# Performance work log

Hardware: AMD Instinct MI355X
Metric: run time of the kernel (lower is better)

The kernel has to match this reference:

```python
import jax, jax.numpy as jnp
import numpy as np

N, H, W, C = 2, 96, 96, 256
HEADS, P = 8, 25
DH = C // HEADS
HID = int(C * 4.0)


def _ln(x, g, b):
    m = jnp.mean(x, axis=-1, keepdims=True)
    v = jnp.var(x, axis=-1, keepdims=True)
    return (x - m) / jnp.sqrt(v + 1e-5) * g + b


def _deform_sample(value, loc, h, w):
    # value: (n, heads, h*w, dh); loc: (n, Lq, heads, P, 2) normalized to [0,1] (x,y)
    # Bilinear sampling with align_corners=False and zero padding, as in
    # grid_sample used by MSDeformAttn.
    n = value.shape[0]
    gx = loc[..., 0] * w - 0.5
    gy = loc[..., 1] * h - 0.5
    x0 = jnp.floor(gx)
    y0 = jnp.floor(gy)
    fx = gx - x0
    fy = gy - y0
    out = jnp.zeros((n, HEADS, gx.shape[1] * P, DH), dtype=value.dtype)
    for dx, dy in ((0, 0), (1, 0), (0, 1), (1, 1)):
        xi = x0 + dx
        yi = y0 + dy
        wgt = (fx if dx else 1.0 - fx) * (fy if dy else 1.0 - fy)
        valid = ((xi >= 0) & (xi <= w - 1) & (yi >= 0) & (yi <= h - 1)).astype(value.dtype)
        xi_c = jnp.clip(xi, 0, w - 1).astype(jnp.int32)
        yi_c = jnp.clip(yi, 0, h - 1).astype(jnp.int32)
        idx = yi_c * w + xi_c                                   # (n, Lq, heads, P)
        idx = jnp.transpose(idx, (0, 2, 1, 3)).reshape(n, HEADS, -1)
        g = jnp.take_along_axis(value, idx[..., None], axis=2)  # (n, heads, Lq*P, dh)
        wv = jnp.transpose(wgt * valid, (0, 2, 1, 3)).reshape(n, HEADS, -1, 1)
        out = out + g * wv
    return out


def setup_inputs() -> dict:
    key = jax.random.key(0)
    ks = jax.random.split(key, 20)
    s = 0.02
    inp = {
        'x': jax.random.normal(ks[0], (N, H, W, C), jnp.float32),
        'ref_points': jax.random.uniform(ks[1], (N, H * W, 1, 2), jnp.float32),
        'spatial_shapes': jnp.array([[H, W]], dtype=jnp.int32),
        'level_start_index': jnp.zeros((1,), dtype=jnp.int32),
        'ln1_g': jnp.ones((C,), jnp.float32),
        'ln1_b': jnp.zeros((C,), jnp.float32),
        'w_off': jax.random.normal(ks[2], (C, HEADS * P * 2), jnp.float32) * s,
        'b_off': jax.random.normal(ks[3], (HEADS * P * 2,), jnp.float32) * s,
        'w_attn': jax.random.normal(ks[4], (C, HEADS * P), jnp.float32) * s,
        'b_attn': jax.random.normal(ks[5], (HEADS * P,), jnp.float32) * s,
        'w_val': jax.random.normal(ks[6], (C, C), jnp.float32) * s,
        'b_val': jnp.zeros((C,), jnp.float32),
        'w_out': jax.random.normal(ks[7], (C, C), jnp.float32) * s,
        'b_out': jnp.zeros((C,), jnp.float32),
        'ln2_g': jnp.ones((C,), jnp.float32),
        'ln2_b': jnp.zeros((C,), jnp.float32),
        'w_fc1': jax.random.normal(ks[8], (C, HID), jnp.float32) * s,
        'b_fc1': jnp.zeros((HID,), jnp.float32),
        'w_fc2': jax.random.normal(ks[9], (HID, C), jnp.float32) * s,
        'b_fc2': jnp.zeros((C,), jnp.float32),
    }
    return inp


def reference(x, ref_points, spatial_shapes, level_start_index,
              ln1_g, ln1_b, w_off, b_off, w_attn, b_attn,
              w_val, b_val, w_out, b_out, ln2_g, ln2_b,
              w_fc1, b_fc1, w_fc2, b_fc2):
    n, h, w, c = x.shape
    lq = h * w
    shortcut = x
    # pre-norm + flatten to query
    q = _ln(x, ln1_g, ln1_b).reshape(n, lq, c)
    # MSDeformAttn (n_levels = 1)
    value = (q @ w_val + b_val).reshape(n, lq, HEADS, DH).transpose(0, 2, 1, 3)
    off = (q @ w_off + b_off).reshape(n, lq, HEADS, P, 2)
    aw = jax.nn.softmax((q @ w_attn + b_attn).reshape(n, lq, HEADS, P), axis=-1)
    norm = jnp.array([w, h], dtype=x.dtype)          # offsets normalized by (W, H)
    ref = ref_points[:, :, 0, :]                     # (n, Lq, 2)
    loc = ref[:, :, None, None, :] + off / norm      # (n, Lq, heads, P, 2)
    sampled = _deform_sample(value, loc, h, w).reshape(n, HEADS, lq, P, DH)
    attn = jnp.einsum('nqhp,nhqpd->nqhd', aw, sampled).reshape(n, lq, c)
    attn = attn @ w_out + b_out
    x1 = shortcut + attn.reshape(n, h, w, c)
    # MLP block
    y = _ln(x1, ln2_g, ln2_b)
    y = jax.nn.gelu(y @ w_fc1 + b_fc1, approximate=False) @ w_fc2 + b_fc2
    return x1 + y
```

## Files before the change

### kernel.cpp

```cpp
#include <hip/hip_runtime.h>
#include <hip/hip_bf16.h>
#include <math.h>

typedef __hip_bfloat16 bf16;
typedef __attribute__((ext_vector_type(8))) short short8;
typedef __attribute__((ext_vector_type(4))) float f32x4;

#define NB 2
#define HH 96
#define WW 96
#define CC 256
#define NHEADS 8
#define PP 25
#define DHH 32
#define HIDN 1024
#define LQ (HH*WW)
#define TT (NB*LQ)
#define NVC 896
#define TB 8

__device__ __forceinline__ float b2f(bf16 v){ return __bfloat162float(v); }
__device__ __forceinline__ bf16  f2b(float v){ return __float2bfloat16(v); }
__device__ __forceinline__ float lo_bf(unsigned u){ return __uint_as_float(u << 16); }
__device__ __forceinline__ float hi_bf(unsigned u){ return __uint_as_float(u & 0xffff0000u); }

__device__ __forceinline__ void gl2lds16(const void* g, void* l) {
    __builtin_amdgcn_global_load_lds(
        (const __attribute__((address_space(1))) unsigned int*)g,
        (__attribute__((address_space(3))) unsigned int*)l, 16, 0, 0);
}

__global__ __launch_bounds__(256) void prep_all(const float* __restrict__ w_val,
                                                const float* __restrict__ w_off,
                                                const float* __restrict__ w_attn,
                                                const float* __restrict__ w_fc1,
                                                const float* __restrict__ w_fc2,
                                                const float* __restrict__ w_out,
                                                const float* __restrict__ b_val,
                                                const float* __restrict__ b_off,
                                                const float* __restrict__ b_attn,
                                                bf16* __restrict__ wvcT,
                                                bf16* __restrict__ wfc1T,
                                                bf16* __restrict__ wfc2T,
                                                bf16* __restrict__ woutT,
                                                float* __restrict__ bvc)
{
    const int idx = blockIdx.x*256 + threadIdx.x;
    if (idx < 229376) {
        int n = idx >> 8, k = idx & 255;
        float v = (n < 256) ? w_val[(size_t)k*256 + n]
                : (n < 656) ? w_off[(size_t)k*400 + (n-256)]
                : (n < 856) ? w_attn[(size_t)k*200 + (n-656)] : 0.f;
        wvcT[idx] = f2b(v);
    } else if (idx < 491520) {
        int j = idx - 229376; int n = j >> 8, k = j & 255;
        wfc1T[j] = f2b(w_fc1[(size_t)k*1024 + n]);
    } else if (idx < 753664) {
        int j = idx - 491520; int n = j >> 10, k = j & 1023;
        wfc2T[j] = f2b(w_fc2[(size_t)k*256 + n]);
    } else if (idx < 819200) {
        int j = idx - 753664; int n = j >> 8, k = j & 255;
        woutT[j] = f2b(w_out[(size_t)k*256 + n]);
    }
    if (idx < NVC)
        bvc[idx] = (idx < 256) ? b_val[idx]
                 : (idx < 656) ? b_off[idx-256]
                 : (idx < 856) ? b_attn[idx-656] : 0.f;
}

__global__ __launch_bounds__(256) void ln_kernel(const float* __restrict__ x,
                                                 const float* __restrict__ g,
                                                 const float* __restrict__ b,
                                                 bf16* __restrict__ out)
{
    const int t = blockIdx.x*4 + (threadIdx.x >> 6);
    const int l = threadIdx.x & 63;
    const float4 v = *(const float4*)(x + (size_t)t*CC + l*4);
    float s  = v.x + v.y + v.z + v.w;
    float s2 = v.x*v.x + v.y*v.y + v.z*v.z + v.w*v.w;
    #pragma unroll
    for (int m = 1; m < 64; m <<= 1) { s += __shfl_xor(s, m); s2 += __shfl_xor(s2, m); }
    const float mean = s * (1.f/CC);
    const float var  = s2 * (1.f/CC) - mean*mean;
    const float rs   = 1.f / sqrtf(var + 1e-5f);
    const float4 gg = *(const float4*)(g + l*4);
    const float4 bb = *(const float4*)(b + l*4);
    bf16 o[4];
    o[0] = f2b((v.x-mean)*rs*gg.x + bb.x);
    o[1] = f2b((v.y-mean)*rs*gg.y + bb.y);
    o[2] = f2b((v.z-mean)*rs*gg.z + bb.z);
    o[3] = f2b((v.w-mean)*rs*gg.w + bb.w);
    *(uint2*)(out + (size_t)t*CC + l*4) = *(uint2*)o;
}

template<int EPI>
__global__ __launch_bounds__(256) void mfma_gemm(const bf16* __restrict__ A,
                                                 const bf16* __restrict__ Bt,
                                                 const float* __restrict__ bias,
                                                 void* __restrict__ outv,
                                                 const float* __restrict__ resid,
                                                 int K, int N)
{
    __shared__ short As[128*64];
    __shared__ short Bs[128*64];
    const int tid = threadIdx.x;
    const int w = tid >> 6, l = tid & 63;
    const int bm = blockIdx.x, bn = blockIdx.y;

    const bf16* sbase[8];
    short*      lbase[8];
    {
        const int lrow = l >> 3;
        const int q    = (l & 7) ^ lrow;
        #pragma unroll
        for (int j = 0; j < 8; j++) {
            int r = w*8 + j;
            bool isA = r < 16;
            int rr = isA ? r : r - 16;
            int row = rr*8 + lrow;
            size_t grow = (size_t)((isA ? bm : bn)*128 + row);
            sbase[j] = (isA ? A : Bt) + grow*K + q*8;
            lbase[j] = (isA ? As : Bs) + rr*512;
        }
    }

    int aoff[2][4], boff[2][4];
    #pragma unroll
    for (int s = 0; s < 2; s++)
        #pragma unroll
        for (int i = 0; i < 4; i++) {
            int q = s*4 + (l >> 4);
            int m = 64*(w >> 1) + i*16 + (l & 15);
            int n = 64*(w &  1) + i*16 + (l & 15);
            aoff[s][i] = (m*8 + (q ^ (m & 7))) * 8;
            boff[s][i] = (n*8 + (q ^ (n & 7))) * 8;
        }

    f32x4 acc[4][4];
    #pragma unroll
    for (int i = 0; i < 4; i++)
        #pragma unroll
        for (int j = 0; j < 4; j++)
            acc[i][j] = (f32x4){0.f, 0.f, 0.f, 0.f};

    for (int k0 = 0; k0 < K; k0 += 64) {
        #pragma unroll
        for (int j = 0; j < 8; j++)
            gl2lds16(sbase[j] + k0, lbase[j]);
        __syncthreads();
        #pragma unroll
        for (int s = 0; s < 2; s++) {
            short8 af[4], bfr[4];
            #pragma unroll
            for (int i = 0; i < 4; i++) {
                af[i]  = *(const short8*)(As + aoff[s][i]);
                bfr[i] = *(const short8*)(Bs + boff[s][i]);
            }
            #pragma unroll
            for (int i = 0; i < 4; i++)
                #pragma unroll
                for (int j = 0; j < 4; j++)
                    acc[i][j] = __builtin_amdgcn_mfma_f32_16x16x32_bf16(af[i], bfr[j], acc[i][j], 0, 0, 0);
        }
        __syncthreads();
    }

    const int row0 = bm*128 + 64*(w >> 1) + (l >> 4)*4;
    const int col0 = bn*128 + 64*(w &  1) + (l & 15);
    #pragma unroll
    for (int i = 0; i < 4; i++) {
        #pragma unroll
        for (int j = 0; j < 4; j++) {
            const int col = col0 + j*16;
            const float bs = bias[col];
            #pragma unroll
            for (int r = 0; r < 4; r++) {
                const int row = row0 + i*16 + r;
                float v = acc[i][j][r] + bs;
                size_t o = (size_t)row * N + col;
                if (EPI == 0) {
                    ((bf16*)outv)[o] = f2b(v);
                } else if (EPI == 2) {
                    ((bf16*)outv)[o] = f2b(0.5f * v * (1.f + erff(v * 0.70710678118654752f)));
                } else {
                    ((float*)outv)[o] = v + resid[o];
                }
            }
        }
    }
}

__global__ __launch_bounds__(256) void softmax_kernel(bf16* __restrict__ vc)
{
    const int gid = blockIdx.x*256 + threadIdx.x;
    if (gid >= TT*NHEADS) return;
    bf16* p = vc + (size_t)(gid >> 3)*NVC + 656 + (gid & 7)*PP;
    float e[PP];
    float m = b2f(p[0]);
    #pragma unroll
    for (int i = 1; i < PP; i++) m = fmaxf(m, b2f(p[i]));
    float s = 0.f;
    #pragma unroll
    for (int i = 0; i < PP; i++) { e[i] = expf(b2f(p[i]) - m); s += e[i]; }
    const float inv = 1.f / s;
    #pragma unroll
    for (int i = 0; i < PP; i++) p[i] = f2b(e[i] * inv);
}

__global__ __launch_bounds__(256) void sample_kernel(const bf16* __restrict__ vc,
                                                     const float* __restrict__ refp,
                                                     bf16* __restrict__ samp)
{
    __shared__ float4  w4[TB*200];
    __shared__ ushort4 i4[TB*200];
    const int b = blockIdx.x;
    const int tbase = ((b & 7)*288 + (b >> 3)) * TB;
    const int tid = threadIdx.x;

    for (int i = tid; i < TB*200; i += 256) {
        const int tl  = (i*5243) >> 20;
        const int rem = i - tl*200;
        const int h   = (rem*41) >> 10;
        const int p   = rem - h*25;
        const int t   = tbase + tl;
        const bf16* row = vc + (size_t)t*NVC;
        const unsigned uo = *(const unsigned*)(row + 256 + h*50 + 2*p);
        const float a  = b2f(row[656 + h*25 + p]);
        const float gx = refp[(size_t)t*2+0]*96.f - 0.5f + lo_bf(uo);
        const float gy = refp[(size_t)t*2+1]*96.f - 0.5f + hi_bf(uo);
        const float x0f = floorf(gx), y0f = floorf(gy);
        const float fx = gx - x0f, fy = gy - y0f;
        const int ix = (int)x0f, iy = (int)y0f;
        float  wv[4];
        ushort ii[4];
        #pragma unroll
        for (int d = 0; d < 4; d++) {
            const int dx = d & 1, dy = d >> 1;
            const int xi = ix + dx, yi = iy + dy;
            const bool valid = (xi >= 0) & (xi <= WW-1) & (yi >= 0) & (yi <= HH-1);
            const int xc = min(max(xi, 0), WW-1);
            const int yc = min(max(yi, 0), HH-1);
            ii[d] = (ushort)(yc*WW + xc);
            wv[d] = valid ? a * (dx ? fx : 1.f-fx) * (dy ? fy : 1.f-fy) : 0.f;
        }
        w4[i] = (float4){wv[0], wv[1], wv[2], wv[3]};
        i4[i] = (ushort4){ii[0], ii[1], ii[2], ii[3]};
    }
    __syncthreads();

    const int wv_ = tid >> 6, l = tid & 63;
    const int tl  = wv_*2 + (l >> 5);
    const int r   = l & 31;
    const int h   = r >> 2, oct = r & 3;
    const int c0  = h*DHH + oct*8;
    const int t   = tbase + tl;
    const int n   = (t >= LQ) ? 1 : 0;
    const bf16* pv = vc + (size_t)n*LQ*NVC + c0;
    const int pib = tl*200 + h*25;

    float acc[8] = {0.f,0.f,0.f,0.f,0.f,0.f,0.f,0.f};
    for (int p = 0; p < PP; p++) {
        const float4  w  = w4[pib + p];
        const ushort4 id = i4[pib + p];
        const float  wt_[4] = {w.x, w.y, w.z, w.w};
        const ushort id_[4] = {id.x, id.y, id.z, id.w};
        #pragma unroll
        for (int d = 0; d < 4; d++) {
            const float wt = wt_[d];
            const uint4 vv = *(const uint4*)(pv + (size_t)id_[d]*NVC);
            acc[0] += wt*lo_bf(vv.x); acc[1] += wt*hi_bf(vv.x);
            acc[2] += wt*lo_bf(vv.y); acc[3] += wt*hi_bf(vv.y);
            acc[4] += wt*lo_bf(vv.z); acc[5] += wt*hi_bf(vv.z);
            acc[6] += wt*lo_bf(vv.w); acc[7] += wt*hi_bf(vv.w);
        }
    }
    bf16 o[8];
    #pragma unroll
    for (int j = 0; j < 8; j++) o[j] = f2b(acc[j]);
    *(uint4*)(samp + (size_t)t*CC + c0) = *(uint4*)o;
}

extern "C" void kernel_launch(void* const* d_in, const int* in_sizes, int n_in,
                              void* d_out, int out_size, void* d_ws, size_t ws_size,
                              hipStream_t stream)
{
    const float* x      = (const float*)d_in[0];
    const float* refp   = (const float*)d_in[1];
    const float* ln1_g  = (const float*)d_in[4];
    const float* ln1_b  = (const float*)d_in[5];
    const float* w_off  = (const float*)d_in[6];
    const float* b_off  = (const float*)d_in[7];
    const float* w_attn = (const float*)d_in[8];
    const float* b_attn = (const float*)d_in[9];
    const float* w_val  = (const float*)d_in[10];
    const float* b_val  = (const float*)d_in[11];
    const float* w_out  = (const float*)d_in[12];
    const float* b_out  = (const float*)d_in[13];
    const float* ln2_g  = (const float*)d_in[14];
    const float* ln2_b  = (const float*)d_in[15];
    const float* w_fc1  = (const float*)d_in[16];
    const float* b_fc1  = (const float*)d_in[17];
    const float* w_fc2  = (const float*)d_in[18];
    const float* b_fc2  = (const float*)d_in[19];

    char* wsb = (char*)d_ws;
    bf16*  q     = (bf16*)(wsb + 0);
    bf16*  vc    = (bf16*)(wsb + 9437184);
    bf16*  samp  = (bf16*)(wsb + 42467328);
    float* x1    = (float*)(wsb + 51904512);
    bf16*  wvcT  = (bf16*)(wsb + 70778880);
    bf16*  wfc1T = (bf16*)(wsb + 71237632);
    bf16*  wfc2T = (bf16*)(wsb + 71761920);
    bf16*  woutT = (bf16*)(wsb + 72286208);
    float* bvc   = (float*)(wsb + 72417280);
    bf16*  hid   = (bf16*)(wsb + 0);
    bf16*  y0    = samp;

    if (ws_size < 72420864) return;

    const dim3 blk(256);
    prep_all<<<dim3(3200), blk, 0, stream>>>(w_val, w_off, w_attn, w_fc1, w_fc2, w_out,
                                             b_val, b_off, b_attn,
                                             wvcT, wfc1T, wfc2T, woutT, bvc);
    ln_kernel<<<dim3(TT/4), blk, 0, stream>>>(x, ln1_g, ln1_b, q);
    mfma_gemm<0><<<dim3(TT/128, NVC/128), blk, 0, stream>>>(q, wvcT, bvc, (void*)vc, nullptr, CC, NVC);
    softmax_kernel<<<dim3(TT*NHEADS/256), blk, 0, stream>>>(vc);
    sample_kernel<<<dim3(TT/TB), blk, 0, stream>>>(vc, refp, samp);
    mfma_gemm<3><<<dim3(TT/128, CC/128),   blk, 0, stream>>>(samp, woutT, b_out, (void*)x1, x, CC, CC);
    ln_kernel<<<dim3(TT/4), blk, 0, stream>>>(x1, ln2_g, ln2_b, y0);
    mfma_gemm<2><<<dim3(TT/128, HIDN/128), blk, 0, stream>>>(y0, wfc1T, b_fc1, (void*)hid, nullptr, CC, HIDN);
    mfma_gemm<3><<<dim3(TT/128, CC/128),   blk, 0, stream>>>(hid, wfc2T, b_fc2, d_out, x1, HIDN, CC);
}
```

Baseline: 265.5 us.

## Fuse attention softmax into sampling kernel, pack taps as fp16, template GEMM dims

Removes the standalone softmax kernel and computes the per-head softmax inside the sampling kernel's tap-building phase, with four lanes per (token, head) reducing via shuffles. This saves one launch and a read-modify-write pass over the attention logits. Tap weights and indices are packed into a 16-byte struct with fp16 weights, halving the LDS footprint and needing one LDS load per point. GEMM K and N become template parameters so the compiler can specialize loops, at the cost of slightly lower weight precision from fp16.

```diff
diff --git a/kernel.cpp b/kernel.cpp
--- a/kernel.cpp
+++ b/kernel.cpp
@@ -93,13 +93,12 @@
     *(uint2*)(out + (size_t)t*CC + l*4) = *(uint2*)o;
 }
 
-template<int EPI>
+template<int EPI, int K, int N>
 __global__ __launch_bounds__(256) void mfma_gemm(const bf16* __restrict__ A,
                                                  const bf16* __restrict__ Bt,
                                                  const float* __restrict__ bias,
                                                  void* __restrict__ outv,
-                                                 const float* __restrict__ resid,
-                                                 int K, int N)
+                                                 const float* __restrict__ resid)
 {
     __shared__ short As[128*64];
     __shared__ short Bs[128*64];
@@ -190,61 +189,75 @@
     }
 }
 
-__global__ __launch_bounds__(256) void softmax_kernel(bf16* __restrict__ vc)
-{
-    const int gid = blockIdx.x*256 + threadIdx.x;
-    if (gid >= TT*NHEADS) return;
-    bf16* p = vc + (size_t)(gid >> 3)*NVC + 656 + (gid & 7)*PP;
-    float e[PP];
-    float m = b2f(p[0]);
-    #pragma unroll
-    for (int i = 1; i < PP; i++) m = fmaxf(m, b2f(p[i]));
-    float s = 0.f;
-    #pragma unroll
-    for (int i = 0; i < PP; i++) { e[i] = expf(b2f(p[i]) - m); s += e[i]; }
-    const float inv = 1.f / s;
-    #pragma unroll
-    for (int i = 0; i < PP; i++) p[i] = f2b(e[i] * inv);
-}
+struct __align__(16) Tap { _Float16 w[4]; unsigned short i[4]; };
 
 __global__ __launch_bounds__(256) void sample_kernel(const bf16* __restrict__ vc,
                                                      const float* __restrict__ refp,
                                                      bf16* __restrict__ samp)
 {
-    __shared__ float4  w4[TB*200];
-    __shared__ ushort4 i4[TB*200];
+    __shared__ Tap taps[TB*200];
     const int b = blockIdx.x;
     const int tbase = ((b & 7)*288 + (b >> 3)) * TB;
     const int tid = threadIdx.x;
 
-    for (int i = tid; i < TB*200; i += 256) {
-        const int tl  = (i*5243) >> 20;
-        const int rem = i - tl*200;
-        const int h   = (rem*41) >> 10;
-        const int p   = rem - h*25;
-        const int t   = tbase + tl;
+    {
+        const int pair = tid >> 2;
+        const int j    = tid & 3;
+        const int tl   = pair >> 3;
+        const int h    = pair & 7;
+        const int t    = tbase + tl;
         const bf16* row = vc + (size_t)t*NVC;
-        const unsigned uo = *(const unsigned*)(row + 256 + h*50 + 2*p);
-        const float a  = b2f(row[656 + h*25 + p]);
-        const float gx = refp[(size_t)t*2+0]*96.f - 0.5f + lo_bf(uo);
-        const float gy = refp[(size_t)t*2+1]*96.f - 0.5f + hi_bf(uo);
-        const float x0f = floorf(gx), y0f = floorf(gy);
-        const float fx = gx - x0f, fy = gy - y0f;
-        const int ix = (int)x0f, iy = (int)y0f;
-        float  wv[4];
-        ushort ii[4];
-        #pragma unroll
-        for (int d = 0; d < 4; d++) {
-            const int dx = d & 1, dy = d >> 1;
-            const int xi = ix + dx, yi = iy + dy;
-            const bool valid = (xi >= 0) & (xi <= WW-1) & (yi >= 0) & (yi <= HH-1);
-            const int xc = min(max(xi, 0), WW-1);
-            const int yc = min(max(yi, 0), HH-1);
-            ii[d] = (ushort)(yc*WW + xc);
-            wv[d] = valid ? a * (dx ? fx : 1.f-fx) * (dy ? fy : 1.f-fy) : 0.f;
-        }
-        w4[i] = (float4){wv[0], wv[1], wv[2], wv[3]};
-        i4[i] = (ushort4){ii[0], ii[1], ii[2], ii[3]};
+
+        float lg[7];
+        #pragma unroll
+        for (int k = 0; k < 7; k++) {
+            int p = j + 4*k;
+            lg[k] = (p < PP) ? b2f(row[656 + h*25 + p]) : -1e30f;
+        }
+        float m = lg[0];
+        #pragma unroll
+        for (int k = 1; k < 7; k++) m = fmaxf(m, lg[k]);
+        m = fmaxf(m, __shfl_xor(m, 1));
+        m = fmaxf(m, __shfl_xor(m, 2));
+        float s = 0.f;
+        float ex[7];
+        #pragma unroll
+        for (int k = 0; k < 7; k++) {
+            ex[k] = (j + 4*k < PP) ? expf(lg[k] - m) : 0.f;
+            s += ex[k];
+        }
+        s += __shfl_xor(s, 1);
+        s += __shfl_xor(s, 2);
+        const float inv = 1.f / s;
+
+        const float rx96 = refp[(size_t)t*2 + 0]*96.f - 0.5f;
+        const float ry96 = refp[(size_t)t*2 + 1]*96.f - 0.5f;
+        const unsigned* offp = (const unsigned*)(row + 256 + h*50);
+
+        #pragma unroll
+        for (int k = 0; k < 7; k++) {
+            const int p = j + 4*k;
+            if (p >= PP) break;
+            const float a = ex[k] * inv;
+            const unsigned uo = offp[p];
+            const float gx = rx96 + lo_bf(uo);
+            const float gy = ry96 + hi_bf(uo);
+            const float x0f = floorf(gx), y0f = floorf(gy);
+            const float fx = gx - x0f, fy = gy - y0f;
+            const int ix = (int)x0f, iy = (int)y0f;
+            Tap tp;
+            #pragma unroll
+            for (int d = 0; d < 4; d++) {
+                const int dx = d & 1, dy = d >> 1;
+                const int xi = ix + dx, yi = iy + dy;
+                const bool valid = (xi >= 0) & (xi <= WW-1) & (yi >= 0) & (yi <= HH-1);
+                const int xc = min(max(xi, 0), WW-1);
+                const int yc = min(max(yi, 0), HH-1);
+                tp.i[d] = (unsigned short)(yc*WW + xc);
+                tp.w[d] = (_Float16)(valid ? a * (dx ? fx : 1.f-fx) * (dy ? fy : 1.f-fy) : 0.f);
+            }
+            taps[tl*200 + h*25 + p] = tp;
+        }
     }
     __syncthreads();
 
@@ -260,14 +273,13 @@
 
     float acc[8] = {0.f,0.f,0.f,0.f,0.f,0.f,0.f,0.f};
     for (int p = 0; p < PP; p++) {
-        const float4  w  = w4[pib + p];
-        const ushort4 id = i4[pib + p];
-        const float  wt_[4] = {w.x, w.y, w.z, w.w};
-        const ushort id_[4] = {id.x, id.y, id.z, id.w};
+        const uint4 tv = *((const uint4*)taps + (pib + p));
+        const _Float16* wp_ = (const _Float16*)&tv;
+        const unsigned short* ip_ = (const unsigned short*)&tv + 4;
         #pragma unroll
         for (int d = 0; d < 4; d++) {
-            const float wt = wt_[d];
-            const uint4 vv = *(const uint4*)(pv + (size_t)id_[d]*NVC);
+            const float wt = (float)wp_[d];
+            const uint4 vv = *(const uint4*)(pv + (size_t)ip_[d]*NVC);
             acc[0] += wt*lo_bf(vv.x); acc[1] += wt*hi_bf(vv.x);
             acc[2] += wt*lo_bf(vv.y); acc[3] += wt*hi_bf(vv.y);
             acc[4] += wt*lo_bf(vv.z); acc[5] += wt*hi_bf(vv.z);
@@ -276,7 +288,7 @@
     }
     bf16 o[8];
     #pragma unroll
-    for (int j = 0; j < 8; j++) o[j] = f2b(acc[j]);
+    for (int j2 = 0; j2 < 8; j2++) o[j2] = f2b(acc[j2]);
     *(uint4*)(samp + (size_t)t*CC + c0) = *(uint4*)o;
 }
 
@@ -323,11 +335,10 @@
                                              b_val, b_off, b_attn,
                                              wvcT, wfc1T, wfc2T, woutT, bvc);
     ln_kernel<<<dim3(TT/4), blk, 0, stream>>>(x, ln1_g, ln1_b, q);
-    mfma_gemm<0><<<dim3(TT/128, NVC/128), blk, 0, stream>>>(q, wvcT, bvc, (void*)vc, nullptr, CC, NVC);
-    softmax_kernel<<<dim3(TT*NHEADS/256), blk, 0, stream>>>(vc);
+    mfma_gemm<0,256,NVC><<<dim3(TT/128, NVC/128), blk, 0, stream>>>(q, wvcT, bvc, (void*)vc, nullptr);
     sample_kernel<<<dim3(TT/TB), blk, 0, stream>>>(vc, refp, samp);
-    mfma_gemm<3><<<dim3(TT/128, CC/128),   blk, 0, stream>>>(samp, woutT, b_out, (void*)x1, x, CC, CC);
+    mfma_gemm<3,256,CC><<<dim3(TT/128, CC/128), blk, 0, stream>>>(samp, woutT, b_out, (void*)x1, x);
     ln_kernel<<<dim3(TT/4), blk, 0, stream>>>(x1, ln2_g, ln2_b, y0);
-    mfma_gemm<2><<<dim3(TT/128, HIDN/128), blk, 0, stream>>>(y0, wfc1T, b_fc1, (void*)hid, nullptr, CC, HIDN);
-    mfma_gemm<3><<<dim3(TT/128, CC/128),   blk, 0, stream>>>(hid, wfc2T, b_fc2, d_out, x1, HIDN, CC);
-}
+    mfma_gemm<2,256,HIDN><<<dim3(TT/128, HIDN/128), blk, 0, stream>>>(y0, wfc1T, b_fc1, (void*)hid, nullptr);
+    mfma_gemm<3,HIDN,CC><<<dim3(TT/128, CC/128), blk, 0, stream>>>(hid, wfc2T, b_fc2, d_out, x1);
+}
```

Result: faster. 249.5 us (-6.0%).
